# Kernel optimization log

Hardware: AMD Instinct MI355X
Metric: run time of the kernel (lower is better)

## Reference

```python
import jax, jax.numpy as jnp
import numpy as np

NEG = -1e9


def setup_inputs() -> dict:
    key = jax.random.key(0)
    ks = jax.random.split(key, 5)
    B, N, D = 2, 1024, 40
    x = jax.random.normal(ks[0], (B, N, D), dtype=jnp.float32)
    # Linear(2D->D): store as (2D, D) so y = cat @ W1 + b1 (transposed torch layout)
    W1 = jax.random.normal(ks[1], (2 * D, D), dtype=jnp.float32) * (1.0 / np.sqrt(2 * D))
    b1 = jax.random.normal(ks[2], (D,), dtype=jnp.float32) * 0.01
    W2 = jax.random.normal(ks[3], (D, D), dtype=jnp.float32) * (1.0 / np.sqrt(D))
    b2 = jax.random.normal(ks[4], (D,), dtype=jnp.float32) * 0.01
    return {"x": x, "W1": W1, "b1": b1, "W2": W2, "b2": b2}


def reference(x, W1, b1, W2, b2):
    B, N, D = x.shape
    # cat([xi, xj]) @ W1 == xi @ W1[:D] + xj @ W1[D:] -> avoid (B,N,N,2D) materialization
    ai = x @ W1[:D]          # (B, N, D), contribution of row index i
    aj = x @ W1[D:]          # (B, N, D), contribution of col index j
    h = jax.nn.gelu(ai[:, :, None, :] + aj[:, None, :, :] + b1, approximate=False)  # (B,N,N,D)
    p = h @ W2 + b2          # (B, N, N, D)
    mask = jnp.triu(jnp.ones((N, N), dtype=bool), 1)  # True where j > i (masked out)
    p = jnp.where(mask[None, :, :, None], 0.0, p)
    sq = jnp.sum(p * p, axis=-1)                       # (B, N, N)
    s = jnp.sqrt(jnp.where(mask[None], 1.0, sq))       # safe sqrt at masked zeros
    s = jnp.where(mask[None], NEG, s)
    w = jax.nn.softmax(s, axis=-1)                     # softmax over j
    return jnp.sum(w[..., None] * p, axis=2)           # (B, N, D)
```

## Files before the change

### kernel.cpp

```cpp
#include <hip/hip_runtime.h>
#include <math.h>

#define D 40
#define NN 1024
#define BB 2

typedef __attribute__((ext_vector_type(8))) _Float16 f16x8;
typedef __attribute__((ext_vector_type(4))) float f32x4;

__device__ __forceinline__ unsigned int pk16(float a, float b) {
    return __builtin_bit_cast(unsigned int, __builtin_amdgcn_cvt_pkrtz(a, b));
}

__device__ __forceinline__ float gelu_tanh(float a) {
    float u = a * a;
    float t1 = fmaf(0.10294366f, u, 2.3022083f);
    float e = __builtin_amdgcn_exp2f(a * t1);
    float r = __builtin_amdgcn_rcpf(e + 1.0f);
    return fmaf(-a, r, a);
}

__device__ __forceinline__ void pinf(float& x) { asm volatile("" : "+v"(x)); }
__device__ __forceinline__ void pin4(float4& v) {
    asm volatile("" : "+v"(v.x), "+v"(v.y), "+v"(v.z), "+v"(v.w));
}
__device__ __forceinline__ void pin8(f16x8& v) {
    uint4 u = __builtin_bit_cast(uint4, v);
    asm volatile("" : "+v"(u.x), "+v"(u.y), "+v"(u.z), "+v"(u.w));
    v = __builtin_bit_cast(f16x8, u);
}

__device__ __forceinline__ f16x8 frag8(float4 a0, float4 a1, float4 x0, float4 x1) {
    float g0 = gelu_tanh(a0.x + x0.x);
    float g1 = gelu_tanh(a0.y + x0.y);
    float g2 = gelu_tanh(a0.z + x0.z);
    float g3 = gelu_tanh(a0.w + x0.w);
    float g4 = gelu_tanh(a1.x + x1.x);
    float g5 = gelu_tanh(a1.y + x1.y);
    float g6 = gelu_tanh(a1.z + x1.z);
    float g7 = gelu_tanh(a1.w + x1.w);
    return __builtin_bit_cast(f16x8,
        make_uint4(pk16(g0, g1), pk16(g2, g3), pk16(g4, g5), pk16(g6, g7)));
}

__global__ __launch_bounds__(64) void precompute_kernel(
    const float* __restrict__ x, const float* __restrict__ W1,
    const float* __restrict__ b1, const float* __restrict__ W2,
    float* __restrict__ ai, float* __restrict__ aj, uint4* __restrict__ w2fT) {
    int r = blockIdx.x;
    int t = threadIdx.x;
    __shared__ float xr[D];
    if (t < D) xr[t] = x[(size_t)r * D + t];
    __syncthreads();
    if (t < D) {
        float s1 = b1[t];
        float s2 = 0.0f;
#pragma unroll
        for (int k = 0; k < D; ++k) {
            float xv = xr[k];
            s1 = fmaf(xv, W1[k * D + t], s1);
            s2 = fmaf(xv, W1[(D + k) * D + t], s2);
        }
        ai[(size_t)r * D + t] = s1;
        aj[(size_t)r * D + t] = s2;
    }
    if (r == 0) {
        const int lr = t & 15, lg = t >> 4;
#pragma unroll
        for (int mt = 0; mt < 3; ++mt)
#pragma unroll
            for (int kt = 0; kt < 2; ++kt) {
                unsigned int u[4];
#pragma unroll
                for (int pe = 0; pe < 4; ++pe) {
                    int k0 = kt * 32 + lg * 8 + pe * 2;
                    int dd = mt * 16 + lr;
                    float v0 = (k0 < D && dd < D) ? W2[k0 * D + dd] : 0.0f;
                    float v1 = (k0 + 1 < D && dd < D) ? W2[(k0 + 1) * D + dd] : 0.0f;
                    u[pe] = pk16(v0, v1);
                }
                w2fT[(mt * 2 + kt) * 64 + t] = make_uint4(u[0], u[1], u[2], u[3]);
            }
    }
}

__global__ __launch_bounds__(256)
__attribute__((amdgpu_waves_per_eu(4)))
void pair_kernel(
    const float* __restrict__ ai_g, const float* __restrict__ aj_g,
    const uint4* __restrict__ w2fT, const float* __restrict__ b2,
    float* __restrict__ out) {
    __shared__ float mbuf[224];

    const int t = threadIdx.x;
    const int bid = blockIdx.x;
    const int bb = bid & 1;
    const int i = NN - 1 - (bid >> 1);
    const int w = t >> 6;
    const int l = t & 63;
    const int lr = l & 15;
    const int lg = l >> 4;
    const int jlo = l & 31;
    const int kk = (l >> 5) << 2;

    f16x8 w2t[3][2];
#pragma unroll
    for (int mt = 0; mt < 3; ++mt)
#pragma unroll
        for (int kt = 0; kt < 2; ++kt) {
            w2t[mt][kt] = __builtin_bit_cast(f16x8, w2fT[(mt * 2 + kt) * 64 + l]);
            pin8(w2t[mt][kt]);
        }

    float bv2[3][4];
#pragma unroll
    for (int mt = 0; mt < 3; ++mt)
#pragma unroll
        for (int r = 0; r < 4; ++r) {
            int d = mt * 16 + lg * 4 + r;
            bv2[mt][r] = (d < D) ? b2[d] : 0.0f;
            pinf(bv2[mt][r]);
        }

    const float* ai_row = ai_g + ((size_t)bb * NN + i) * D;
    float4 air0 = *reinterpret_cast<const float4*>(ai_row + (lg << 3));
    float4 air1 = *reinterpret_cast<const float4*>(ai_row + (lg << 3) + 4);
    float4 ai32 = *reinterpret_cast<const float4*>(ai_row + 32 + kk);
    pin4(air0); pin4(air1); pin4(ai32);

    const float* aj_b = aj_g + (size_t)bb * NN * D;

    float m_run = 0.0f, l_run = 0.0f;
    float o[3][4];
#pragma unroll
    for (int mt = 0; mt < 3; ++mt)
#pragma unroll
        for (int r = 0; r < 4; ++r) o[mt][r] = 0.0f;

    for (int jbase = w << 5; jbase <= i; jbase += 128) {
        float4 qa0, qa1, qb0, qb1, qt;
        {
            const int j0 = min(jbase + lr, i);
            const float* r0 = aj_b + (size_t)j0 * D + (lg << 3);
            qa0 = *reinterpret_cast<const float4*>(r0);
            qa1 = *reinterpret_cast<const float4*>(r0 + 4);
            const int j1 = min(jbase + 16 + lr, i);
            const float* r1 = aj_b + (size_t)j1 * D + (lg << 3);
            qb0 = *reinterpret_cast<const float4*>(r1);
            qb1 = *reinterpret_cast<const float4*>(r1 + 4);
            const int jt = min(jbase + jlo, i);
            qt = *reinterpret_cast<const float4*>(aj_b + (size_t)jt * D + 32 + kk);
        }

        unsigned int pd0, pd1;
        {
            float g0 = gelu_tanh(ai32.x + qt.x);
            float g1 = gelu_tanh(ai32.y + qt.y);
            float g2 = gelu_tanh(ai32.z + qt.z);
            float g3 = gelu_tanh(ai32.w + qt.w);
            pd0 = pk16(g0, g1);
            pd1 = pk16(g2, g3);
        }
        const int idx0 = lr << 2;
        uint4 tB0, tB1;
        tB0.x = __builtin_amdgcn_ds_bpermute(idx0,       pd0);
        tB0.y = __builtin_amdgcn_ds_bpermute(idx0,       pd1);
        tB0.z = __builtin_amdgcn_ds_bpermute(idx0 + 128, pd0);
        tB0.w = __builtin_amdgcn_ds_bpermute(idx0 + 128, pd1);
        tB1.x = __builtin_amdgcn_ds_bpermute(idx0 + 64,  pd0);
        tB1.y = __builtin_amdgcn_ds_bpermute(idx0 + 64,  pd1);
        tB1.z = __builtin_amdgcn_ds_bpermute(idx0 + 192, pd0);
        tB1.w = __builtin_amdgcn_ds_bpermute(idx0 + 192, pd1);

        f32x4 acc[3][2];
#pragma unroll
        for (int mt = 0; mt < 3; ++mt)
#pragma unroll
            for (int n = 0; n < 2; ++n)
                acc[mt][n] = (f32x4){bv2[mt][0], bv2[mt][1], bv2[mt][2], bv2[mt][3]};

        {
            f16x8 B = frag8(air0, air1, qa0, qa1);
            f16x8 Bt = __builtin_bit_cast(f16x8, tB0);
#pragma unroll
            for (int mt = 0; mt < 3; ++mt) {
                acc[mt][0] = __builtin_amdgcn_mfma_f32_16x16x32_f16(
                    w2t[mt][0], B, acc[mt][0], 0, 0, 0);
                acc[mt][0] = __builtin_amdgcn_mfma_f32_16x16x32_f16(
                    w2t[mt][1], Bt, acc[mt][0], 0, 0, 0);
            }
        }
        {
            f16x8 B = frag8(air0, air1, qb0, qb1);
            f16x8 Bt = __builtin_bit_cast(f16x8, tB1);
#pragma unroll
            for (int mt = 0; mt < 3; ++mt) {
                acc[mt][1] = __builtin_amdgcn_mfma_f32_16x16x32_f16(
                    w2t[mt][0], B, acc[mt][1], 0, 0, 0);
                acc[mt][1] = __builtin_amdgcn_mfma_f32_16x16x32_f16(
                    w2t[mt][1], Bt, acc[mt][1], 0, 0, 0);
            }
        }

        float sv[2];
#pragma unroll
        for (int n = 0; n < 2; ++n) {
            float sq = 0.0f;
#pragma unroll
            for (int mt = 0; mt < 3; ++mt)
#pragma unroll
                for (int r = 0; r < 4; ++r)
                    sq = fmaf(acc[mt][n][r], acc[mt][n][r], sq);
            sq += __shfl_xor(sq, 16);
            sq += __shfl_xor(sq, 32);
            int j = jbase + n * 16 + lr;
            sv[n] = (j <= i) ? __builtin_amdgcn_sqrtf(sq) : -1e30f;
        }
        float mx = fmaxf(sv[0], sv[1]);
        mx = fmaxf(mx, __shfl_xor(mx, 1));
        mx = fmaxf(mx, __shfl_xor(mx, 2));
        mx = fmaxf(mx, __shfl_xor(mx, 4));
        mx = fmaxf(mx, __shfl_xor(mx, 8));
        if (mx > m_run) {
            float scale = __expf(m_run - mx);
            l_run *= scale;
#pragma unroll
            for (int mt = 0; mt < 3; ++mt)
#pragma unroll
                for (int r = 0; r < 4; ++r) o[mt][r] *= scale;
            m_run = mx;
        }
        float w0 = __expf(sv[0] - m_run);
        float w1 = __expf(sv[1] - m_run);
        l_run += w0 + w1;
#pragma unroll
        for (int mt = 0; mt < 3; ++mt)
#pragma unroll
            for (int r = 0; r < 4; ++r)
                o[mt][r] = fmaf(w0, acc[mt][0][r], fmaf(w1, acc[mt][1][r], o[mt][r]));
    }

#pragma unroll
    for (int mt = 0; mt < 3; ++mt)
#pragma unroll
        for (int r = 0; r < 4; ++r) {
            float v = o[mt][r];
            v += __shfl_xor(v, 1);
            v += __shfl_xor(v, 2);
            v += __shfl_xor(v, 4);
            v += __shfl_xor(v, 8);
            o[mt][r] = v;
        }
    l_run += __shfl_xor(l_run, 1);
    l_run += __shfl_xor(l_run, 2);
    l_run += __shfl_xor(l_run, 4);
    l_run += __shfl_xor(l_run, 8);

    if (lr == 0) {
#pragma unroll
        for (int mt = 0; mt < 3; ++mt)
#pragma unroll
            for (int r = 0; r < 4; ++r) {
                int d = mt * 16 + lg * 4 + r;
                if (d < D) mbuf[w * 56 + d] = o[mt][r];
            }
        if (lg == 0) { mbuf[w * 56 + 48] = l_run; mbuf[w * 56 + 49] = m_run; }
    }
    __syncthreads();
    if (t < D) {
        float M = fmaxf(fmaxf(mbuf[49], mbuf[56 + 49]),
                        fmaxf(mbuf[112 + 49], mbuf[168 + 49]));
        float L = 0.0f, val = 0.0f;
#pragma unroll
        for (int ww = 0; ww < 4; ++ww) {
            float c = __expf(mbuf[ww * 56 + 49] - M);
            L = fmaf(c, mbuf[ww * 56 + 48], L);
            val = fmaf(c, mbuf[ww * 56 + t], val);
        }
        out[((size_t)bb * NN + i) * D + t] = val / L;
    }
}

extern "C" void kernel_launch(void* const* d_in, const int* in_sizes, int n_in,
                              void* d_out, int out_size, void* d_ws, size_t ws_size,
                              hipStream_t stream) {
    const float* x  = (const float*)d_in[0];
    const float* W1 = (const float*)d_in[1];
    const float* b1 = (const float*)d_in[2];
    const float* W2 = (const float*)d_in[3];
    const float* b2 = (const float*)d_in[4];
    float* out = (float*)d_out;

    float* ai = (float*)d_ws;
    float* aj = ai + (size_t)BB * NN * D;
    uint4* w2fT = (uint4*)(aj + (size_t)BB * NN * D);

    precompute_kernel<<<BB * NN, 64, 0, stream>>>(x, W1, b1, W2, ai, aj, w2fT);
    pair_kernel<<<BB * NN, 256, 0, stream>>>(ai, aj, w2fT, b2, out);
}
```

Baseline: 35.17 us.

## Software-pipeline aj loads, defer softmax max reduction, remap tail-column loads

The j-loop is restructured into a two-stage ping-pong so the aj loads for the next 128-column step are issued before the current step is computed, hiding global-load latency. The per-iteration cross-lane max reduction is removed: each lane keeps its own running max and rescales only when the new max exceeds it by a margin, and the lane maxima are reconciled once after the loop. The tail-column (d 32..39) load now reuses the row pointers already computed for the main fragments, and waves_per_eu is lowered from 4 to 3 to leave room for the extra live registers. The lazy rescale lets exp arguments reach the margin, which bounds overflow risk but changes rounding slightly, and lower occupancy may reduce latency hiding elsewhere.

After: 35.26 us. Within noise of the previous version (+0.2%).

```diff
diff --git a/kernel.cpp b/kernel.cpp
--- a/kernel.cpp
+++ b/kernel.cpp
@@ -85,7 +85,7 @@
 }
 
 __global__ __launch_bounds__(256)
-__attribute__((amdgpu_waves_per_eu(4)))
+__attribute__((amdgpu_waves_per_eu(3)))
 void pair_kernel(
     const float* __restrict__ ai_g, const float* __restrict__ aj_g,
     const uint4* __restrict__ w2fT, const float* __restrict__ b2,
@@ -100,8 +100,6 @@
     const int l = t & 63;
     const int lr = l & 15;
     const int lg = l >> 4;
-    const int jlo = l & 31;
-    const int kk = (l >> 5) << 2;
 
     f16x8 w2t[3][2];
 #pragma unroll
@@ -125,7 +123,7 @@
     const float* ai_row = ai_g + ((size_t)bb * NN + i) * D;
     float4 air0 = *reinterpret_cast<const float4*>(ai_row + (lg << 3));
     float4 air1 = *reinterpret_cast<const float4*>(ai_row + (lg << 3) + 4);
-    float4 ai32 = *reinterpret_cast<const float4*>(ai_row + 32 + kk);
+    float4 ai32 = *reinterpret_cast<const float4*>(ai_row + 32 + ((lg >> 1) << 2));
     pin4(air0); pin4(air1); pin4(ai32);
 
     const float* aj_b = aj_g + (size_t)bb * NN * D;
@@ -137,21 +135,21 @@
 #pragma unroll
         for (int r = 0; r < 4; ++r) o[mt][r] = 0.0f;
 
-    for (int jbase = w << 5; jbase <= i; jbase += 128) {
-        float4 qa0, qa1, qb0, qb1, qt;
-        {
-            const int j0 = min(jbase + lr, i);
-            const float* r0 = aj_b + (size_t)j0 * D + (lg << 3);
-            qa0 = *reinterpret_cast<const float4*>(r0);
-            qa1 = *reinterpret_cast<const float4*>(r0 + 4);
-            const int j1 = min(jbase + 16 + lr, i);
-            const float* r1 = aj_b + (size_t)j1 * D + (lg << 3);
-            qb0 = *reinterpret_cast<const float4*>(r1);
-            qb1 = *reinterpret_cast<const float4*>(r1 + 4);
-            const int jt = min(jbase + jlo, i);
-            qt = *reinterpret_cast<const float4*>(aj_b + (size_t)jt * D + 32 + kk);
-        }
-
+    auto ldq = [&](int jbase, float4& qa0, float4& qa1, float4& qb0,
+                   float4& qb1, float4& qt) {
+        const int j0 = min(jbase + lr, i);
+        const int j1 = min(jbase + 16 + lr, i);
+        const float* r0 = aj_b + (size_t)j0 * D;
+        const float* r1 = aj_b + (size_t)j1 * D;
+        qa0 = *reinterpret_cast<const float4*>(r0 + (lg << 3));
+        qa1 = *reinterpret_cast<const float4*>(r0 + (lg << 3) + 4);
+        qb0 = *reinterpret_cast<const float4*>(r1 + (lg << 3));
+        qb1 = *reinterpret_cast<const float4*>(r1 + (lg << 3) + 4);
+        qt  = *reinterpret_cast<const float4*>(((lg & 1) ? r1 : r0) + 32 + ((lg >> 1) << 2));
+    };
+
+    auto compute = [&](int jbase, float4 qa0, float4 qa1, float4 qb0,
+                       float4 qb1, float4 qt) {
         unsigned int pd0, pd1;
         {
             float g0 = gelu_tanh(ai32.x + qt.x);
@@ -178,7 +176,6 @@
 #pragma unroll
             for (int n = 0; n < 2; ++n)
                 acc[mt][n] = (f32x4){bv2[mt][0], bv2[mt][1], bv2[mt][2], bv2[mt][3]};
-
         {
             f16x8 B = frag8(air0, air1, qa0, qa1);
             f16x8 Bt = __builtin_bit_cast(f16x8, tB0);
@@ -217,11 +214,7 @@
             sv[n] = (j <= i) ? __builtin_amdgcn_sqrtf(sq) : -1e30f;
         }
         float mx = fmaxf(sv[0], sv[1]);
-        mx = fmaxf(mx, __shfl_xor(mx, 1));
-        mx = fmaxf(mx, __shfl_xor(mx, 2));
-        mx = fmaxf(mx, __shfl_xor(mx, 4));
-        mx = fmaxf(mx, __shfl_xor(mx, 8));
-        if (mx > m_run) {
+        if (mx > m_run + 8.0f) {
             float scale = __expf(m_run - mx);
             l_run *= scale;
 #pragma unroll
@@ -238,13 +231,34 @@
 #pragma unroll
             for (int r = 0; r < 4; ++r)
                 o[mt][r] = fmaf(w0, acc[mt][0][r], fmaf(w1, acc[mt][1][r], o[mt][r]));
-    }
-
+    };
+
+    float4 Aq0, Aq1, Aq2, Aq3, Aqt, Bq0, Bq1, Bq2, Bq3, Bqt;
+    const int jb0 = w << 5;
+    if (jb0 <= i) {
+        ldq(jb0, Aq0, Aq1, Aq2, Aq3, Aqt);
+        for (int jbase = jb0; jbase <= i; jbase += 256) {
+            ldq(jbase + 128, Bq0, Bq1, Bq2, Bq3, Bqt);
+            compute(jbase, Aq0, Aq1, Aq2, Aq3, Aqt);
+            if (jbase + 128 <= i) {
+                ldq(jbase + 256, Aq0, Aq1, Aq2, Aq3, Aqt);
+                compute(jbase + 128, Bq0, Bq1, Bq2, Bq3, Bqt);
+            }
+        }
+    }
+
+    float M = m_run;
+    M = fmaxf(M, __shfl_xor(M, 1));
+    M = fmaxf(M, __shfl_xor(M, 2));
+    M = fmaxf(M, __shfl_xor(M, 4));
+    M = fmaxf(M, __shfl_xor(M, 8));
+    float c0 = __expf(m_run - M);
+    l_run *= c0;
 #pragma unroll
     for (int mt = 0; mt < 3; ++mt)
 #pragma unroll
         for (int r = 0; r < 4; ++r) {
-            float v = o[mt][r];
+            float v = o[mt][r] * c0;
             v += __shfl_xor(v, 1);
             v += __shfl_xor(v, 2);
             v += __shfl_xor(v, 4);
@@ -264,16 +278,16 @@
                 int d = mt * 16 + lg * 4 + r;
                 if (d < D) mbuf[w * 56 + d] = o[mt][r];
             }
-        if (lg == 0) { mbuf[w * 56 + 48] = l_run; mbuf[w * 56 + 49] = m_run; }
+        if (lg == 0) { mbuf[w * 56 + 48] = l_run; mbuf[w * 56 + 49] = M; }
     }
     __syncthreads();
     if (t < D) {
-        float M = fmaxf(fmaxf(mbuf[49], mbuf[56 + 49]),
-                        fmaxf(mbuf[112 + 49], mbuf[168 + 49]));
+        float Mg = fmaxf(fmaxf(mbuf[49], mbuf[56 + 49]),
+                         fmaxf(mbuf[112 + 49], mbuf[168 + 49]));
         float L = 0.0f, val = 0.0f;
 #pragma unroll
         for (int ww = 0; ww < 4; ++ww) {
-            float c = __expf(mbuf[ww * 56 + 49] - M);
+            float c = __expf(mbuf[ww * 56 + 49] - Mg);
             L = fmaf(c, mbuf[ww * 56 + 48], L);
             val = fmaf(c, mbuf[ww * 56 + t], val);
         }
```
